# Kernel tuning notes

Hardware: AMD Instinct MI355X
Metric: run time of the kernel (lower is better)

The kernel has to match this reference:

```python
import jax, jax.numpy as jnp
import numpy as np

DIM = 256
HEADS = 8
HD = DIM // HEADS          # 32
WS = 8                     # window size
TOPK = 4
SCALE = HD ** -0.5


def setup_inputs() -> dict:
    key = jax.random.key(0)
    k1, k2, k3 = jax.random.split(key, 3)
    B, H, W = 8, 64, 64
    x = jax.random.normal(k1, (B, DIM, H, W), dtype=jnp.float32)
    # 1x1 conv weights (BN folded -> weight + bias), fan-in scaled to keep logits sane
    w_qkv = jax.random.normal(k2, (3 * DIM, DIM), dtype=jnp.float32) / np.sqrt(DIM)
    b_qkv = jnp.zeros((3 * DIM,), dtype=jnp.float32)
    w_proj = jax.random.normal(k3, (DIM, DIM), dtype=jnp.float32) / np.sqrt(DIM)
    b_proj = jnp.zeros((DIM,), dtype=jnp.float32)
    return {"x": x, "w_qkv": w_qkv, "b_qkv": b_qkv, "w_proj": w_proj, "b_proj": b_proj}


def _window_partition(t, ws):
    # t: [BH, D, H, W] -> [BH, R, ws*ws, D]
    bh, d, h, w = t.shape
    gh, gw = h // ws, w // ws
    t = t.reshape(bh, d, gh, ws, gw, ws)
    t = t.transpose(0, 2, 4, 3, 5, 1)          # [BH, gh, gw, ws, ws, D]
    return t.reshape(bh, gh * gw, ws * ws, d)


def reference(x, w_qkv, b_qkv, w_proj, b_proj):
    B, C, H, W = x.shape
    gh, gw = H // WS, W // WS
    R, T = gh * gw, WS * WS
    BH = B * HEADS

    # qkv 1x1 conv
    qkv = jnp.einsum('bchw,oc->bohw', x, w_qkv) + b_qkv[None, :, None, None]
    q, k, v = jnp.split(qkv, 3, axis=1)                       # each [B, C, H, W]

    def to_bh(t):
        return t.reshape(BH, HD, H, W)

    q_w = _window_partition(to_bh(q), WS)                     # [BH, R, T, HD]
    k_w = _window_partition(to_bh(k), WS)
    v_w = _window_partition(to_bh(v), WS)

    # region-level routing: mean-pooled region tokens
    q_r = q_w.mean(axis=2)                                    # [BH, R, HD]
    k_r = k_w.mean(axis=2)
    attn_r = jnp.einsum('brd,bkd->brk', q_r, k_r) * SCALE     # [BH, R, R]
    topk = min(TOPK, R)
    _, topk_idx = jax.lax.top_k(attn_r, topk)                 # [BH, R, K]

    # gather top-k key/value windows per query region
    bidx = jnp.arange(BH)[:, None, None]
    k_sel = k_w[bidx, topk_idx]                               # [BH, R, K, T, HD]
    v_sel = v_w[bidx, topk_idx]
    k_sel = k_sel.reshape(BH, R, topk * T, HD)
    v_sel = v_sel.reshape(BH, R, topk * T, HD)

    # token-level attention inside routed regions
    attn = jnp.einsum('brtd,brsd->brts', q_w, k_sel) * SCALE  # [BH, R, T, K*T]
    attn = jax.nn.softmax(attn, axis=-1)
    out_w = jnp.einsum('brts,brsd->brtd', attn, v_sel)        # [BH, R, T, HD]

    # window reverse -> [BH, HD, H, W]
    out = out_w.reshape(BH, gh, gw, WS, WS, HD)
    out = out.transpose(0, 5, 1, 3, 2, 4).reshape(BH, HD, H, W)
    out = out.reshape(B, C, H, W)

    out = jnp.einsum('bchw,oc->bohw', out, w_proj) + b_proj[None, :, None, None]
    return out
```

## Files before the change

kernel.cpp:

```cpp
#include <hip/hip_runtime.h>
#include <hip/hip_bf16.h>

#define ATT_SCALE 0.17677669529663687f
#define EXP_C1 0.2550349235534668f
#define EXP_C2 23.083120654223400f

typedef short v8s __attribute__((ext_vector_type(8)));
typedef float v4f __attribute__((ext_vector_type(4)));
typedef float v16f __attribute__((ext_vector_type(16)));
typedef const __attribute__((address_space(1))) unsigned int gu32;
typedef __attribute__((address_space(3))) unsigned int lu32;

__device__ __forceinline__ void g2l16(const void* g, void* l) {
  __builtin_amdgcn_global_load_lds((gu32*)g, (lu32*)l, 16, 0, 0);
}

__device__ __forceinline__ float bflo(unsigned u){ union{unsigned i;float f;}x; x.i=u<<16; return x.f; }
__device__ __forceinline__ float bfhi(unsigned u){ union{unsigned i;float f;}x; x.i=u&0xffff0000u; return x.f; }
__device__ __forceinline__ unsigned short bf16r(float v){
  __hip_bfloat16 h = __float2bfloat16(v);
  return *reinterpret_cast<unsigned short*>(&h);
}
__device__ __forceinline__ unsigned pack_bf2(float a, float b){
  return (unsigned)bf16r(a) | ((unsigned)bf16r(b) << 16);
}
__device__ __forceinline__ unsigned cvtpk(float lo, float hi){
  unsigned r;
  asm("v_cvt_pk_bf16_f32 %0, %1, %2" : "=v"(r) : "v"(lo), "v"(hi));
  return r;
}
__device__ __forceinline__ void pl32swap(unsigned &a, unsigned &b){
  asm volatile("v_permlane32_swap_b32 %0, %1" : "+v"(a), "+v"(b));
}

__global__ __launch_bounds__(256) void k_prep(const float* __restrict__ x,
                                              const float* __restrict__ w_qkv,
                                              const float* __restrict__ w_proj,
                                              unsigned short* __restrict__ Xb,
                                              unsigned short* __restrict__ Wq,
                                              unsigned short* __restrict__ Wp,
                                              float* __restrict__ part) {
  __shared__ __align__(16) char hbuf[8192];
  __shared__ float pbuf[512];
  const int blk = blockIdx.x;
  const int t = threadIdx.x;
  if (blk >= 2048) {
    const int m = blk - 2048;
    const float* src = (m < 768) ? (w_qkv + m*256) : (w_proj + (size_t)(m - 768)*256);
    unsigned short* dst = (m < 768) ? (Wq + m*256) : (Wp + (size_t)(m - 768)*256);
    int col = (t & ~63) | ((t & 63) ^ ((m & 7) << 3));
    dst[col] = bf16r(src[t]);
    return;
  }
  const int b = blk >> 8, cc = (blk >> 6) & 3, pc = blk & 63;
  const int c0 = cc << 6, p0 = pc << 6;
  const int wv = t >> 6, lane = t & 63;

  float hi[16];
  const float* xp = x + ((size_t)(b*256 + c0 + wv*16))*4096 + p0 + lane;
  #pragma unroll
  for (int i = 0; i < 16; ++i) hi[i] = xp[(size_t)i*4096];

  #pragma unroll
  for (int i = 0; i < 16; ++i) {
    float s = hi[i];
    s += __shfl_xor(s, 1);
    s += __shfl_xor(s, 2);
    s += __shfl_xor(s, 4);
    if ((lane & 7) == 0) pbuf[(wv*16 + i)*8 + (lane >> 3)] = s;
  }

  #pragma unroll
  for (int gi = 0; gi < 2; ++gi) {
    uint4 uh;
    uh.x = pack_bf2(hi[gi*8+0], hi[gi*8+1]); uh.y = pack_bf2(hi[gi*8+2], hi[gi*8+3]);
    uh.z = pack_bf2(hi[gi*8+4], hi[gi*8+5]); uh.w = pack_bf2(hi[gi*8+6], hi[gi*8+7]);
    int off = lane*128 + ((wv*32 + gi*16) ^ ((lane & 7) << 4));
    *(uint4*)(hbuf + off) = uh;
  }
  __syncthreads();
  const size_t rowbase = ((size_t)(b*4096 + p0)) * 512 + (size_t)c0*2;
  #pragma unroll
  for (int s = 0; s < 2; ++s) {
    int gidx = s*256 + t;
    int row = gidx >> 3, gb = (gidx & 7) << 4;
    uint4 vh = *(const uint4*)(hbuf + row*128 + gb);
    *(uint4*)((char*)Xb + rowbase + (size_t)row*512 + gb) = vh;
  }
  const size_t pbase = ((size_t)(b*64 + pc)*256 + c0)*8;
  part[pbase + t]       = pbuf[t];
  part[pbase + 256 + t] = pbuf[t + 256];
}

__global__ __launch_bounds__(256) void k_xmr(const float* __restrict__ part,
                                             float* __restrict__ xmean) {
  const int blk = blockIdx.x;
  const int item = blk & 7;
  const int b = blk >> 6, rh = (blk >> 3) & 7;
  const int t = threadIdx.x;
  const int flat = item*256 + t;
  float acc = 0.f;
  const float* pp = part + (size_t)(b*64 + rh*8)*2048 + flat;
  #pragma unroll
  for (int j = 0; j < 8; ++j) acc += pp[(size_t)j*2048];
  const int c = flat >> 3, wc = flat & 7;
  xmean[(size_t)((b*256 + c) << 6) + (rh << 3) + wc] = acc * 0.015625f;
}

__global__ __launch_bounds__(256) void k_route(const float* __restrict__ xmean,
                                               const float* __restrict__ w_qkv,
                                               const float* __restrict__ b_qkv,
                                               int* __restrict__ topk) {
  __shared__ float xm[128][64];
  __shared__ float qr[64][33];
  __shared__ float kr[64][33];
  const int bh = blockIdx.x, b = bh >> 3, head = bh & 7;
  const int tid = threadIdx.x;
  const int d = tid & 31, r0 = tid >> 5;
  float qacc[8], kacc[8];
  const float bq = b_qkv[head*32 + d], bk = b_qkv[256 + head*32 + d];
  #pragma unroll
  for (int i = 0; i < 8; ++i) { qacc[i] = bq; kacc[i] = bk; }

  for (int c0 = 0; c0 < 256; c0 += 128) {
    __syncthreads();
    #pragma unroll
    for (int i = 0; i < 32; ++i) {
      int idx = i*256 + tid;
      int row = idx >> 6, col = idx & 63;
      xm[row][col] = xmean[(size_t)(b*256 + c0 + row)*64 + col];
    }
    __syncthreads();
    const float* wqp = w_qkv + (head*32 + d)*256 + c0;
    const float* wkp = w_qkv + (256 + head*32 + d)*256 + c0;
    for (int c = 0; c < 128; ++c) {
      float wq = wqp[c], wk = wkp[c];
      #pragma unroll
      for (int i = 0; i < 8; ++i) {
        float xv = xm[c][r0 + 8*i];
        qacc[i] += wq * xv;
        kacc[i] += wk * xv;
      }
    }
  }
  #pragma unroll
  for (int i = 0; i < 8; ++i) { qr[r0+8*i][d] = qacc[i]; kr[r0+8*i][d] = kacc[i]; }
  __syncthreads();

  float* ar = &xm[0][0];
  for (int item = tid; item < 4096; item += 256) {
    int i = item >> 6, j = item & 63;
    float s = 0.f;
    #pragma unroll
    for (int dd = 0; dd < 32; ++dd) s += qr[i][dd]*kr[j][dd];
    ar[i*64 + j] = s;
  }
  __syncthreads();
  if (tid < 64) {
    for (int kk = 0; kk < 4; ++kk) {
      float best = -3e38f; int bj = 0;
      for (int j = 0; j < 64; ++j) {
        float v = ar[tid*64 + j];
        if (v > best) { best = v; bj = j; }
      }
      ar[tid*64 + bj] = -3e38f;
      topk[(bh*64 + tid)*4 + kk] = bj;
    }
  }
}

template<int EPI>
__global__ __launch_bounds__(256) void k_gemm(
    const unsigned short* __restrict__ Wstk,
    const unsigned short* __restrict__ Bmat,
    const float* __restrict__ bias,
    unsigned short* __restrict__ qbuf, unsigned short* __restrict__ kbuf,
    unsigned short* __restrict__ vbuf, float* __restrict__ outp) {
  __shared__ __align__(16) char lds[40960];
  const int tid = threadIdx.x;
  const int wv = tid >> 6, lane = tid & 63;
  const int nt = blockIdx.x, mt = blockIdx.y;

  v4f acc[4][4];
  #pragma unroll
  for (int i = 0; i < 4; ++i)
    #pragma unroll
    for (int j = 0; j < 4; ++j) acc[i][j] = (v4f){0.f,0.f,0.f,0.f};

  const char* wlanebase = (const char*)Wstk + ((size_t)(mt*256) + (lane>>3))*512 + (lane&7)*16;
  const size_t prowlane = (size_t)(nt*64 + (lane>>3))*512 + (lane&7)*16;

  for (int kt = 0; kt < 4; ++kt) {
    const int k0b = kt * 128;
    __syncthreads();
    #pragma unroll
    for (int o = 0; o < 8; ++o) {
      int op = wv*8 + o;
      g2l16(wlanebase + (size_t)(op*8)*512 + k0b, lds + op*1024);
    }
    #pragma unroll
    for (int o = 0; o < 2; ++o) {
      int op = wv*2 + o;
      g2l16((const char*)Bmat + prowlane + (size_t)(op*8)*512 + k0b, lds + 32768 + op*1024);
    }
    __syncthreads();
    #pragma unroll
    for (int kk = 0; kk < 2; ++kk) {
      const int kb = kk*64 + ((lane>>4)<<4);
      v8s a[4], b[4];
      #pragma unroll
      for (int i = 0; i < 4; ++i) {
        int mr = wv*64 + i*16 + (lane & 15);
        a[i] = *(const v8s*)(lds + mr*128 + (kb ^ ((mr & 7) << 4)));
      }
      #pragma unroll
      for (int j = 0; j < 4; ++j) {
        int nr = j*16 + (lane & 15);
        b[j] = *(const v8s*)(lds + 32768 + nr*128 + (kb ^ ((nr & 7) << 4)));
      }
      #pragma unroll
      for (int i = 0; i < 4; ++i)
        #pragma unroll
        for (int j = 0; j < 4; ++j)
          acc[i][j] = __builtin_amdgcn_mfma_f32_16x16x32_bf16(a[i], b[j], acc[i][j], 0, 0, 0);
    }
  }

  if (EPI == 0) {
    if (mt < 2) {
      unsigned short* outbuf = (mt == 0) ? qbuf : kbuf;
      #pragma unroll
      for (int i = 0; i < 4; ++i) {
        int o = mt*256 + wv*64 + i*16 + ((lane >> 4) << 2);
        int head = (o >> 5) & 7, d0 = o & 31;
        float b0 = bias[o], b1 = bias[o+1], b2 = bias[o+2], b3 = bias[o+3];
        #pragma unroll
        for (int j = 0; j < 4; ++j) {
          int p = nt*64 + j*16 + (lane & 15);
          int bb = p >> 12, ploc = p & 4095;
          int h = ploc >> 6, w = ploc & 63;
          int rr = ((h >> 3) << 3) | (w >> 3), tt = ((h & 7) << 3) | (w & 7);
          int bh = bb*8 + head;
          uint2 u;
          u.x = pack_bf2(acc[i][j][0] + b0, acc[i][j][1] + b1);
          u.y = pack_bf2(acc[i][j][2] + b2, acc[i][j][3] + b3);
          *(uint2*)(outbuf + (size_t)(((bh << 6) | rr)*64 + tt)*32 + d0) = u;
        }
      }
    } else {
      #pragma unroll
      for (int i = 0; i < 4; ++i) {
        int o = 512 + wv*64 + i*16 + ((lane >> 4) << 2);
        int vch = o - 512;
        int head = vch >> 5, d0 = vch & 31;
        float bv[4] = {bias[o], bias[o+1], bias[o+2], bias[o+3]};
        #pragma unroll
        for (int j = 0; j < 4; ++j) {
          int p = nt*64 + j*16 + (lane & 15);
          int bb = p >> 12, ploc = p & 4095;
          int h = ploc >> 6, w = ploc & 63;
          int rr = ((h >> 3) << 3) | (w >> 3), tt = ((h & 7) << 3) | (w & 7);
          int bh = bb*8 + head;
          size_t base = ((size_t)((bh << 6) | rr)*32 + d0)*64 + tt;
          #pragma unroll
          for (int c = 0; c < 4; ++c)
            vbuf[base + (size_t)c*64] = bf16r(acc[i][j][c] + bv[c]);
        }
      }
    }
  } else {
    #pragma unroll
    for (int i = 0; i < 4; ++i) {
      int o = wv*64 + i*16 + ((lane >> 4) << 2);
      float b0 = bias[o], b1 = bias[o+1], b2 = bias[o+2], b3 = bias[o+3];
      #pragma unroll
      for (int j = 0; j < 4; ++j) {
        int p = nt*64 + j*16 + (lane & 15);
        int bb = p >> 12, ploc = p & 4095;
        float* dst = outp + ((size_t)(bb*256 + o))*4096 + ploc;
        dst[0]     = acc[i][j][0] + b0;
        dst[4096]  = acc[i][j][1] + b1;
        dst[8192]  = acc[i][j][2] + b2;
        dst[12288] = acc[i][j][3] + b3;
      }
    }
  }
}

__global__ __launch_bounds__(256) void k_attn(const unsigned short* __restrict__ qw,
                                              const unsigned short* __restrict__ kw,
                                              const unsigned short* __restrict__ vwt,
                                              const int* __restrict__ topk,
                                              unsigned short* __restrict__ owt) {
  const int lane = threadIdx.x & 63;
  const int W = blockIdx.x*4 + (threadIdx.x >> 6);
  const int bh = W >> 6, rr = W & 63;
  const int lo5 = lane & 31, hi = lane >> 5;
  const int b = bh >> 3, head = bh & 7;

  const unsigned short* qb = qw + (size_t)(bh*64 + rr)*2048;
  v8s qf[2][2];
  #pragma unroll
  for (int qt = 0; qt < 2; ++qt)
    #pragma unroll
    for (int ck = 0; ck < 2; ++ck)
      qf[qt][ck] = *(const v8s*)(qb + (qt*32 + lo5)*32 + ck*16 + hi*8);

  int idx4[4];
  #pragma unroll
  for (int w = 0; w < 4; ++w) idx4[w] = topk[(bh*64 + rr)*4 + w];

  v16f O[2];
  #pragma unroll
  for (int qt = 0; qt < 2; ++qt)
    #pragma unroll
    for (int r = 0; r < 16; ++r) O[qt][r] = 0.f;
  float lsum[2] = {0.f, 0.f};

  #pragma unroll
  for (int w = 0; w < 4; ++w) {
    const unsigned short* kb = kw  + (size_t)(bh*64 + idx4[w])*2048;
    const unsigned short* vb = vwt + (size_t)(bh*64 + idx4[w])*2048;
    v8s kf[2][2], vf[4];
    #pragma unroll
    for (int kt = 0; kt < 2; ++kt)
      #pragma unroll
      for (int ck = 0; ck < 2; ++ck)
        kf[kt][ck] = *(const v8s*)(kb + (kt*32 + lo5)*32 + ck*16 + hi*8);
    #pragma unroll
    for (int mk = 0; mk < 4; ++mk)
      vf[mk] = *(const v8s*)(vb + lo5*64 + mk*16 + hi*8);

    v16f S[2][2];
    #pragma unroll
    for (int kt = 0; kt < 2; ++kt)
      #pragma unroll
      for (int qt = 0; qt < 2; ++qt) {
        v16f z;
        #pragma unroll
        for (int r = 0; r < 16; ++r) z[r] = 0.f;
        z = __builtin_amdgcn_mfma_f32_32x32x16_bf16(kf[kt][0], qf[qt][0], z, 0, 0, 0);
        S[kt][qt] = __builtin_amdgcn_mfma_f32_32x32x16_bf16(kf[kt][1], qf[qt][1], z, 0, 0, 0);
      }

    #pragma unroll
    for (int kt = 0; kt < 2; ++kt) {
      #pragma unroll
      for (int qt = 0; qt < 2; ++qt) {
        float p[16];
        #pragma unroll
        for (int r = 0; r < 16; ++r)
          p[r] = __builtin_amdgcn_exp2f(__builtin_fmaf(S[kt][qt][r], EXP_C1, -EXP_C2));
        float s01 = (p[0]+p[1]) + (p[2]+p[3]);
        float s23 = (p[4]+p[5]) + (p[6]+p[7]);
        float s45 = (p[8]+p[9]) + (p[10]+p[11]);
        float s67 = (p[12]+p[13]) + (p[14]+p[15]);
        lsum[qt] += (s01 + s23) + (s45 + s67);

        unsigned wh[8], wl[8];
        #pragma unroll
        for (int i = 0; i < 8; ++i) {
          wh[i] = cvtpk(p[2*i], p[2*i+1]);
          float l0 = p[2*i]   - bflo(wh[i]);
          float l1 = p[2*i+1] - bfhi(wh[i]);
          wl[i] = cvtpk(l0, l1);
        }
        pl32swap(wh[0], wh[2]); pl32swap(wh[1], wh[3]);
        pl32swap(wh[4], wh[6]); pl32swap(wh[5], wh[7]);
        pl32swap(wl[0], wl[2]); pl32swap(wl[1], wl[3]);
        pl32swap(wl[4], wl[6]); pl32swap(wl[5], wl[7]);
        union { unsigned u[4]; v8s v; } fA, fB;
        fA.u[0] = wh[0]; fA.u[1] = wh[1]; fA.u[2] = wh[2]; fA.u[3] = wh[3];
        fB.u[0] = wl[0]; fB.u[1] = wl[1]; fB.u[2] = wl[2]; fB.u[3] = wl[3];
        O[qt] = __builtin_amdgcn_mfma_f32_32x32x16_bf16(fA.v, vf[2*kt], O[qt], 0, 0, 0);
        O[qt] = __builtin_amdgcn_mfma_f32_32x32x16_bf16(fB.v, vf[2*kt], O[qt], 0, 0, 0);
        fA.u[0] = wh[4]; fA.u[1] = wh[5]; fA.u[2] = wh[6]; fA.u[3] = wh[7];
        fB.u[0] = wl[4]; fB.u[1] = wl[5]; fB.u[2] = wl[6]; fB.u[3] = wl[7];
        O[qt] = __builtin_amdgcn_mfma_f32_32x32x16_bf16(fA.v, vf[2*kt+1], O[qt], 0, 0, 0);
        O[qt] = __builtin_amdgcn_mfma_f32_32x32x16_bf16(fB.v, vf[2*kt+1], O[qt], 0, 0, 0);
      }
    }
  }

  float linv[2];
  #pragma unroll
  for (int qt = 0; qt < 2; ++qt) {
    float t = lsum[qt] + __shfl_xor(lsum[qt], 32);
    linv[qt] = 1.0f / t;
  }

  #pragma unroll
  for (int qt = 0; qt < 2; ++qt) {
    #pragma unroll
    for (int r = 0; r < 16; ++r) {
      int q = (r & 3) + 8*(r >> 2) + 4*hi;
      float li = __shfl(linv[qt], q);
      float val = O[qt][r] * li;
      int tok = qt*32 + q;
      int h = ((rr >> 3) << 3) | (tok >> 3);
      int wcol = ((rr & 7) << 3) | (tok & 7);
      int pg = (b << 12) | (h << 6) | wcol;
      int col = ((head >> 1) << 6) | ((((head & 1) << 5) + lo5) ^ ((tok & 7) << 3));
      owt[(size_t)pg*256 + col] = bf16r(val);
    }
  }
}

extern "C" void kernel_launch(void* const* d_in, const int* in_sizes, int n_in,
                              void* d_out, int out_size, void* d_ws, size_t ws_size,
                              hipStream_t stream) {
  (void)in_sizes; (void)n_in; (void)out_size; (void)ws_size;
  const float* x      = (const float*)d_in[0];
  const float* w_qkv  = (const float*)d_in[1];
  const float* b_qkv  = (const float*)d_in[2];
  const float* w_proj = (const float*)d_in[3];
  const float* b_proj = (const float*)d_in[4];
  float* out = (float*)d_out;

  char* ws = (char*)d_ws;
  unsigned short* Xb  = (unsigned short*)ws;
  unsigned short* Wq  = (unsigned short*)(ws + 16777216);
  unsigned short* Wp  = (unsigned short*)(ws + 17170432);
  unsigned short* qw  = (unsigned short*)(ws + 17301504);
  unsigned short* kw  = (unsigned short*)(ws + 34078720);
  unsigned short* vwt = (unsigned short*)(ws + 50855936);
  float* part         = (float*)(ws + 67633152);
  float* xmean        = (float*)(ws + 71827456);
  int* topk           = (int*)(ws + 72351744);
  unsigned short* owt = Xb;

  k_prep <<<dim3(3072), 256, 0, stream>>>(x, w_qkv, w_proj, Xb, Wq, Wp, part);
  k_xmr  <<<dim3(512),  256, 0, stream>>>(part, xmean);
  k_route<<<dim3(64),   256, 0, stream>>>(xmean, w_qkv, b_qkv, topk);
  k_gemm<0><<<dim3(512, 3), 256, 0, stream>>>(Wq, Xb, b_qkv, qw, kw, vwt, nullptr);
  k_attn <<<dim3(1024), 256, 0, stream>>>(qw, kw, vwt, topk, owt);
  k_gemm<1><<<dim3(512, 1), 256, 0, stream>>>(Wp, owt, b_proj, nullptr, nullptr, nullptr, out);
}
```

Baseline: 119.0 us.

## Fuse x conversion and partial sums into the QKV GEMM kernel

The x-to-bf16 conversion and region partial sums move into a new QKV GEMM kernel. Each block keeps its 64-pixel by 256-channel bf16 tile of x resident in LDS and loops over six 128-row slices of the weight matrix, so the Xb intermediate is never written to or re-read from global memory. Weight conversion becomes its own small kernel. The trade-off is fewer blocks (512 instead of 1536) running longer serial loops, with more LDS per block, which may lower occupancy and latency hiding.

After: 120.7 us. About the same (+1.5%).

```diff
diff --git a/kernel.cpp b/kernel.cpp
--- a/kernel.cpp
+++ b/kernel.cpp
@@ -33,63 +33,146 @@
   asm volatile("v_permlane32_swap_b32 %0, %1" : "+v"(a), "+v"(b));
 }
 
-__global__ __launch_bounds__(256) void k_prep(const float* __restrict__ x,
-                                              const float* __restrict__ w_qkv,
-                                              const float* __restrict__ w_proj,
-                                              unsigned short* __restrict__ Xb,
-                                              unsigned short* __restrict__ Wq,
-                                              unsigned short* __restrict__ Wp,
-                                              float* __restrict__ part) {
-  __shared__ __align__(16) char hbuf[8192];
-  __shared__ float pbuf[512];
-  const int blk = blockIdx.x;
-  const int t = threadIdx.x;
-  if (blk >= 2048) {
-    const int m = blk - 2048;
-    const float* src = (m < 768) ? (w_qkv + m*256) : (w_proj + (size_t)(m - 768)*256);
-    unsigned short* dst = (m < 768) ? (Wq + m*256) : (Wp + (size_t)(m - 768)*256);
-    int col = (t & ~63) | ((t & 63) ^ ((m & 7) << 3));
-    dst[col] = bf16r(src[t]);
-    return;
-  }
-  const int b = blk >> 8, cc = (blk >> 6) & 3, pc = blk & 63;
-  const int c0 = cc << 6, p0 = pc << 6;
-  const int wv = t >> 6, lane = t & 63;
-
-  float hi[16];
-  const float* xp = x + ((size_t)(b*256 + c0 + wv*16))*4096 + p0 + lane;
-  #pragma unroll
-  for (int i = 0; i < 16; ++i) hi[i] = xp[(size_t)i*4096];
-
-  #pragma unroll
-  for (int i = 0; i < 16; ++i) {
-    float s = hi[i];
-    s += __shfl_xor(s, 1);
-    s += __shfl_xor(s, 2);
-    s += __shfl_xor(s, 4);
-    if ((lane & 7) == 0) pbuf[(wv*16 + i)*8 + (lane >> 3)] = s;
-  }
-
-  #pragma unroll
-  for (int gi = 0; gi < 2; ++gi) {
-    uint4 uh;
-    uh.x = pack_bf2(hi[gi*8+0], hi[gi*8+1]); uh.y = pack_bf2(hi[gi*8+2], hi[gi*8+3]);
-    uh.z = pack_bf2(hi[gi*8+4], hi[gi*8+5]); uh.w = pack_bf2(hi[gi*8+6], hi[gi*8+7]);
-    int off = lane*128 + ((wv*32 + gi*16) ^ ((lane & 7) << 4));
-    *(uint4*)(hbuf + off) = uh;
+__global__ __launch_bounds__(256) void k_wprep(const float* __restrict__ w_qkv,
+                                               const float* __restrict__ w_proj,
+                                               unsigned short* __restrict__ Wq,
+                                               unsigned short* __restrict__ Wp) {
+  const int m = blockIdx.x, t = threadIdx.x;
+  const float* src = (m < 768) ? (w_qkv + m*256) : (w_proj + (size_t)(m - 768)*256);
+  unsigned short* dst = (m < 768) ? (Wq + m*256) : (Wp + (size_t)(m - 768)*256);
+  int col = (t & ~63) | ((t & 63) ^ ((m & 7) << 3));
+  dst[col] = bf16r(src[t]);
+}
+
+__global__ __launch_bounds__(256) void k_fqkv(
+    const float* __restrict__ x,
+    const unsigned short* __restrict__ Wq,
+    const float* __restrict__ bias,
+    unsigned short* __restrict__ qbuf, unsigned short* __restrict__ kbuf,
+    unsigned short* __restrict__ vbuf, float* __restrict__ part) {
+  __shared__ __align__(16) char lds[49152];
+  const int tid = threadIdx.x;
+  const int wv = tid >> 6, lane = tid & 63;
+  const int nt = blockIdx.x;
+  const int b = nt >> 6, pc = nt & 63;
+  const int p0 = pc << 6;
+  float* pbuf = (float*)(lds + 32768);
+
+  #pragma unroll
+  for (int cc = 0; cc < 4; ++cc) {
+    float hi[16];
+    const float* xp = x + ((size_t)(b*256 + cc*64 + wv*16))*4096 + p0 + lane;
+    #pragma unroll
+    for (int i = 0; i < 16; ++i) hi[i] = xp[(size_t)i*4096];
+
+    #pragma unroll
+    for (int i = 0; i < 16; ++i) {
+      float s = hi[i];
+      s += __shfl_xor(s, 1);
+      s += __shfl_xor(s, 2);
+      s += __shfl_xor(s, 4);
+      if ((lane & 7) == 0) pbuf[cc*512 + (wv*16 + i)*8 + (lane >> 3)] = s;
+    }
+    #pragma unroll
+    for (int gi = 0; gi < 2; ++gi) {
+      uint4 uh;
+      uh.x = pack_bf2(hi[gi*8+0], hi[gi*8+1]); uh.y = pack_bf2(hi[gi*8+2], hi[gi*8+3]);
+      uh.z = pack_bf2(hi[gi*8+4], hi[gi*8+5]); uh.w = pack_bf2(hi[gi*8+6], hi[gi*8+7]);
+      int off = lane*512 + cc*128 + ((wv*32 + gi*16) ^ ((lane & 7) << 4));
+      *(uint4*)(lds + off) = uh;
+    }
   }
   __syncthreads();
-  const size_t rowbase = ((size_t)(b*4096 + p0)) * 512 + (size_t)c0*2;
-  #pragma unroll
-  for (int s = 0; s < 2; ++s) {
-    int gidx = s*256 + t;
-    int row = gidx >> 3, gb = (gidx & 7) << 4;
-    uint4 vh = *(const uint4*)(hbuf + row*128 + gb);
-    *(uint4*)((char*)Xb + rowbase + (size_t)row*512 + gb) = vh;
-  }
-  const size_t pbase = ((size_t)(b*64 + pc)*256 + c0)*8;
-  part[pbase + t]       = pbuf[t];
-  part[pbase + 256 + t] = pbuf[t + 256];
+  {
+    const size_t pbase = (size_t)(b*64 + pc)*2048;
+    #pragma unroll
+    for (int s = 0; s < 8; ++s) part[pbase + s*256 + tid] = pbuf[s*256 + tid];
+  }
+  __syncthreads();
+
+  const char* wlanebase = (const char*)Wq + ((size_t)(lane >> 3))*512 + (lane & 7)*16;
+
+  #pragma unroll
+  for (int m = 0; m < 6; ++m) {
+    v4f acc[2][4];
+    #pragma unroll
+    for (int i = 0; i < 2; ++i)
+      #pragma unroll
+      for (int j = 0; j < 4; ++j) acc[i][j] = (v4f){0.f,0.f,0.f,0.f};
+
+    #pragma unroll
+    for (int kt = 0; kt < 4; ++kt) {
+      __syncthreads();
+      #pragma unroll
+      for (int o = 0; o < 4; ++o) {
+        int op = wv*4 + o;
+        g2l16(wlanebase + (size_t)(m*128 + op*8)*512 + kt*128, lds + 32768 + op*1024);
+      }
+      __syncthreads();
+      #pragma unroll
+      for (int kk = 0; kk < 2; ++kk) {
+        const int kb = kk*64 + ((lane>>4)<<4);
+        v8s a[2], bfr[4];
+        #pragma unroll
+        for (int i = 0; i < 2; ++i) {
+          int mr = wv*32 + i*16 + (lane & 15);
+          a[i] = *(const v8s*)(lds + 32768 + mr*128 + (kb ^ ((mr & 7) << 4)));
+        }
+        #pragma unroll
+        for (int j = 0; j < 4; ++j) {
+          int nr = j*16 + (lane & 15);
+          bfr[j] = *(const v8s*)(lds + nr*512 + kt*128 + (kb ^ ((nr & 7) << 4)));
+        }
+        #pragma unroll
+        for (int i = 0; i < 2; ++i)
+          #pragma unroll
+          for (int j = 0; j < 4; ++j)
+            acc[i][j] = __builtin_amdgcn_mfma_f32_16x16x32_bf16(a[i], bfr[j], acc[i][j], 0, 0, 0);
+      }
+    }
+
+    if (m < 4) {
+      unsigned short* outbuf = (m < 2) ? qbuf : kbuf;
+      #pragma unroll
+      for (int i = 0; i < 2; ++i) {
+        int o = m*128 + wv*32 + i*16 + ((lane >> 4) << 2);
+        int head = (o >> 5) & 7, d0 = o & 31;
+        float b0 = bias[o], b1 = bias[o+1], b2 = bias[o+2], b3 = bias[o+3];
+        #pragma unroll
+        for (int j = 0; j < 4; ++j) {
+          int p = nt*64 + j*16 + (lane & 15);
+          int bb = p >> 12, ploc = p & 4095;
+          int h = ploc >> 6, w = ploc & 63;
+          int rr = ((h >> 3) << 3) | (w >> 3), tt = ((h & 7) << 3) | (w & 7);
+          int bh = bb*8 + head;
+          uint2 u;
+          u.x = pack_bf2(acc[i][j][0] + b0, acc[i][j][1] + b1);
+          u.y = pack_bf2(acc[i][j][2] + b2, acc[i][j][3] + b3);
+          *(uint2*)(outbuf + (size_t)(((bh << 6) | rr)*64 + tt)*32 + d0) = u;
+        }
+      }
+    } else {
+      #pragma unroll
+      for (int i = 0; i < 2; ++i) {
+        int o = m*128 + wv*32 + i*16 + ((lane >> 4) << 2);
+        int vch = o - 512;
+        int head = vch >> 5, d0 = vch & 31;
+        float bv[4] = {bias[o], bias[o+1], bias[o+2], bias[o+3]};
+        #pragma unroll
+        for (int j = 0; j < 4; ++j) {
+          int p = nt*64 + j*16 + (lane & 15);
+          int bb = p >> 12, ploc = p & 4095;
+          int h = ploc >> 6, w = ploc & 63;
+          int rr = ((h >> 3) << 3) | (w >> 3), tt = ((h & 7) << 3) | (w & 7);
+          int bh = bb*8 + head;
+          size_t base = ((size_t)((bh << 6) | rr)*32 + d0)*64 + tt;
+          #pragma unroll
+          for (int c = 0; c < 4; ++c)
+            vbuf[base + (size_t)c*64] = bf16r(acc[i][j][c] + bv[c]);
+        }
+      }
+    }
+  }
 }
 
 __global__ __launch_bounds__(256) void k_xmr(const float* __restrict__ part,
@@ -169,17 +252,15 @@
   }
 }
 
-template<int EPI>
-__global__ __launch_bounds__(256) void k_gemm(
-    const unsigned short* __restrict__ Wstk,
+__global__ __launch_bounds__(256) void k_proj(
+    const unsigned short* __restrict__ Wp,
     const unsigned short* __restrict__ Bmat,
     const float* __restrict__ bias,
-    unsigned short* __restrict__ qbuf, unsigned short* __restrict__ kbuf,
-    unsigned short* __restrict__ vbuf, float* __restrict__ outp) {
+    float* __restrict__ outp) {
   __shared__ __align__(16) char lds[40960];
   const int tid = threadIdx.x;
   const int wv = tid >> 6, lane = tid & 63;
-  const int nt = blockIdx.x, mt = blockIdx.y;
+  const int nt = blockIdx.x;
 
   v4f acc[4][4];
   #pragma unroll
@@ -187,7 +268,7 @@
     #pragma unroll
     for (int j = 0; j < 4; ++j) acc[i][j] = (v4f){0.f,0.f,0.f,0.f};
 
-  const char* wlanebase = (const char*)Wstk + ((size_t)(mt*256) + (lane>>3))*512 + (lane&7)*16;
+  const char* wlanebase = (const char*)Wp + ((size_t)(lane>>3))*512 + (lane&7)*16;
   const size_t prowlane = (size_t)(nt*64 + (lane>>3))*512 + (lane&7)*16;
 
   for (int kt = 0; kt < 4; ++kt) {
@@ -226,63 +307,19 @@
     }
   }
 
-  if (EPI == 0) {
-    if (mt < 2) {
-      unsigned short* outbuf = (mt == 0) ? qbuf : kbuf;
-      #pragma unroll
-      for (int i = 0; i < 4; ++i) {
-        int o = mt*256 + wv*64 + i*16 + ((lane >> 4) << 2);
-        int head = (o >> 5) & 7, d0 = o & 31;
-        float b0 = bias[o], b1 = bias[o+1], b2 = bias[o+2], b3 = bias[o+3];
-        #pragma unroll
-        for (int j = 0; j < 4; ++j) {
-          int p = nt*64 + j*16 + (lane & 15);
-          int bb = p >> 12, ploc = p & 4095;
-          int h = ploc >> 6, w = ploc & 63;
-          int rr = ((h >> 3) << 3) | (w >> 3), tt = ((h & 7) << 3) | (w & 7);
-          int bh = bb*8 + head;
-          uint2 u;
-          u.x = pack_bf2(acc[i][j][0] + b0, acc[i][j][1] + b1);
-          u.y = pack_bf2(acc[i][j][2] + b2, acc[i][j][3] + b3);
-          *(uint2*)(outbuf + (size_t)(((bh << 6) | rr)*64 + tt)*32 + d0) = u;
-        }
-      }
-    } else {
-      #pragma unroll
-      for (int i = 0; i < 4; ++i) {
-        int o = 512 + wv*64 + i*16 + ((lane >> 4) << 2);
-        int vch = o - 512;
-        int head = vch >> 5, d0 = vch & 31;
-        float bv[4] = {bias[o], bias[o+1], bias[o+2], bias[o+3]};
-        #pragma unroll
-        for (int j = 0; j < 4; ++j) {
-          int p = nt*64 + j*16 + (lane & 15);
-          int bb = p >> 12, ploc = p & 4095;
-          int h = ploc >> 6, w = ploc & 63;
-          int rr = ((h >> 3) << 3) | (w >> 3), tt = ((h & 7) << 3) | (w & 7);
-          int bh = bb*8 + head;
-          size_t base = ((size_t)((bh << 6) | rr)*32 + d0)*64 + tt;
-          #pragma unroll
-          for (int c = 0; c < 4; ++c)
-            vbuf[base + (size_t)c*64] = bf16r(acc[i][j][c] + bv[c]);
-        }
-      }
-    }
-  } else {
-    #pragma unroll
-    for (int i = 0; i < 4; ++i) {
-      int o = wv*64 + i*16 + ((lane >> 4) << 2);
-      float b0 = bias[o], b1 = bias[o+1], b2 = bias[o+2], b3 = bias[o+3];
-      #pragma unroll
-      for (int j = 0; j < 4; ++j) {
-        int p = nt*64 + j*16 + (lane & 15);
-        int bb = p >> 12, ploc = p & 4095;
-        float* dst = outp + ((size_t)(bb*256 + o))*4096 + ploc;
-        dst[0]     = acc[i][j][0] + b0;
-        dst[4096]  = acc[i][j][1] + b1;
-        dst[8192]  = acc[i][j][2] + b2;
-        dst[12288] = acc[i][j][3] + b3;
-      }
+  #pragma unroll
+  for (int i = 0; i < 4; ++i) {
+    int o = wv*64 + i*16 + ((lane >> 4) << 2);
+    float b0 = bias[o], b1 = bias[o+1], b2 = bias[o+2], b3 = bias[o+3];
+    #pragma unroll
+    for (int j = 0; j < 4; ++j) {
+      int p = nt*64 + j*16 + (lane & 15);
+      int bb = p >> 12, ploc = p & 4095;
+      float* dst = outp + ((size_t)(bb*256 + o))*4096 + ploc;
+      dst[0]     = acc[i][j][0] + b0;
+      dst[4096]  = acc[i][j][1] + b1;
+      dst[8192]  = acc[i][j][2] + b2;
+      dst[12288] = acc[i][j][3] + b3;
     }
   }
 }
@@ -418,7 +455,7 @@
   float* out = (float*)d_out;
 
   char* ws = (char*)d_ws;
-  unsigned short* Xb  = (unsigned short*)ws;
+  unsigned short* owt = (unsigned short*)ws;
   unsigned short* Wq  = (unsigned short*)(ws + 16777216);
   unsigned short* Wp  = (unsigned short*)(ws + 17170432);
   unsigned short* qw  = (unsigned short*)(ws + 17301504);
@@ -427,12 +464,11 @@
   float* part         = (float*)(ws + 67633152);
   float* xmean        = (float*)(ws + 71827456);
   int* topk           = (int*)(ws + 72351744);
-  unsigned short* owt = Xb;
-
-  k_prep <<<dim3(3072), 256, 0, stream>>>(x, w_qkv, w_proj, Xb, Wq, Wp, part);
+
+  k_wprep<<<dim3(1024), 256, 0, stream>>>(w_qkv, w_proj, Wq, Wp);
+  k_fqkv <<<dim3(512),  256, 0, stream>>>(x, Wq, b_qkv, qw, kw, vwt, part);
   k_xmr  <<<dim3(512),  256, 0, stream>>>(part, xmean);
   k_route<<<dim3(64),   256, 0, stream>>>(xmean, w_qkv, b_qkv, topk);
-  k_gemm<0><<<dim3(512, 3), 256, 0, stream>>>(Wq, Xb, b_qkv, qw, kw, vwt, nullptr);
   k_attn <<<dim3(1024), 256, 0, stream>>>(qw, kw, vwt, topk, owt);
-  k_gemm<1><<<dim3(512, 1), 256, 0, stream>>>(Wp, owt, b_proj, nullptr, nullptr, nullptr, out);
-}
+  k_proj <<<dim3(512),  256, 0, stream>>>(Wp, owt, b_proj, out);
+}
```
